# Kernel tuning notes

Measured on AMD Instinct MI355X. Metric: run time of the kernel, lower is better.

The kernel has to match this reference:

```python
import jax, jax.numpy as jnp
import numpy as np

N, E = 50000, 800000
IN, C, H, EDIM = 128, 16, 8, 8  # in_channels, out_channels per head, heads, edge_dim
NEG_SLOPE = 0.2


def setup_inputs() -> dict:
    key = jax.random.key(0)
    ks = jax.random.split(key, 10)
    g = 1.0 / np.sqrt(IN)
    inp = {
        "x": jax.random.normal(ks[0], (N, IN), dtype=jnp.float32),
        "edge_index": jax.random.randint(ks[1], (2, E), 0, N, dtype=jnp.int64),
        "edge_attr": jax.random.normal(ks[2], (E, EDIM), dtype=jnp.float32),
        # GATv2Conv params (share_weights=False): lin_l, lin_r with bias, lin_edge no bias
        "W_l": jax.random.normal(ks[3], (IN, H * C), dtype=jnp.float32) * g,
        "b_l": jnp.zeros((H * C,), dtype=jnp.float32),
        "W_r": jax.random.normal(ks[4], (IN, H * C), dtype=jnp.float32) * g,
        "b_r": jnp.zeros((H * C,), dtype=jnp.float32),
        "W_e": jax.random.normal(ks[5], (EDIM, H * C), dtype=jnp.float32) * (1.0 / np.sqrt(EDIM)),
        "att": jax.random.normal(ks[6], (H, C), dtype=jnp.float32) * (1.0 / np.sqrt(C)),
        "bias": jnp.zeros((H * C,), dtype=jnp.float32),
    }
    return inp


def _gatv2_forward(x, edge_index, edge_attr, W_l, b_l, W_r, b_r, W_e, att, bias):
    n = x.shape[0]
    x_l = (x @ W_l + b_l).reshape(n, H, C)  # source transform
    x_r = (x @ W_r + b_r).reshape(n, H, C)  # target transform

    # add self-loops; edge_attr fill_value='mean' (PyG GATv2Conv default)
    loop = jnp.arange(n, dtype=edge_index.dtype)
    src = jnp.concatenate([edge_index[0], loop])
    dst = jnp.concatenate([edge_index[1], loop])
    loop_attr = jnp.broadcast_to(edge_attr.mean(axis=0, keepdims=True), (n, EDIM))
    e_attr = jnp.concatenate([edge_attr, loop_attr], axis=0)  # [E+N, EDIM]

    e_emb = (e_attr @ W_e).reshape(-1, H, C)  # [E+N, H, C]
    m = x_l[src] + x_r[dst] + e_emb          # gather per edge
    m = jax.nn.leaky_relu(m, NEG_SLOPE)
    logit = jnp.einsum("ehc,hc->eh", m, att)  # [E+N, H]

    # destination-grouped (scatter) softmax
    seg_max = jax.ops.segment_max(logit, dst, num_segments=n)
    expd = jnp.exp(logit - seg_max[dst])
    seg_sum = jax.ops.segment_sum(expd, dst, num_segments=n)
    alpha = expd / (seg_sum[dst] + 1e-16)     # [E+N, H]

    msg = alpha[:, :, None] * x_l[src]        # [E+N, H, C]
    out = jax.ops.segment_sum(msg, dst, num_segments=n)  # [N, H, C]
    return out.reshape(n, H * C) + bias       # concat heads + bias


def reference(x, edge_index, edge_attr, W_l, b_l, W_r, b_r, W_e, att, bias):
    return _gatv2_forward(x, edge_index, edge_attr, W_l, b_l, W_r, b_r, W_e, att, bias)
```

## Files before the change

### kernel.cpp

```cpp
#include <hip/hip_runtime.h>

#define NHEAD 8
#define CH    16
#define HC    128
#define INC   128
#define EDIM  8
#define NEG   0.2f

typedef _Float16 h8 __attribute__((ext_vector_type(8)));
typedef _Float16 h4 __attribute__((ext_vector_type(4)));
typedef _Float16 h2 __attribute__((ext_vector_type(2)));
typedef float    f4 __attribute__((ext_vector_type(4)));

__device__ __forceinline__ float lrelu(float v) { return v > 0.f ? v : NEG * v; }

__global__ void k_loop_emb(const float* __restrict__ attr_sum, const float* __restrict__ We,
                           const float* __restrict__ att, float* __restrict__ loop_emb,
                           _Float16* __restrict__ We16, _Float16* __restrict__ att16,
                           float invE) {
    int j = threadIdx.x;
    float acc = 0.f;
    #pragma unroll
    for (int d = 0; d < EDIM; ++d) {
        float w = We[d * HC + j];
        acc += attr_sum[d] * invE * w;
        We16[d * HC + j] = (_Float16)w;
    }
    loop_emb[j] = acc;
    att16[j] = (_Float16)att[j];
}

__global__ void k_packW(const float* __restrict__ Wl, const float* __restrict__ Wr,
                        _Float16* __restrict__ packed) {
    int id = blockIdx.x * blockDim.x + threadIdx.x;
    int l  = id & 63;
    int kb = (id >> 6) & 3;
    int t  = id >> 8;
    int col = t * 16 + (l & 15);
    const float* W = (col < HC) ? Wl : Wr;
    int c = col & 127;
    int kbase = kb * 32 + (l >> 4) * 8;
    _Float16* dst = packed + (size_t)id * 8;
    #pragma unroll
    for (int j = 0; j < 8; ++j) dst[j] = (_Float16)W[(size_t)(kbase + j) * HC + c];
}

__global__ __launch_bounds__(256) void k_gemm_mfma(
        const float* __restrict__ x, const _Float16* __restrict__ packed,
        const float* __restrict__ bl, const float* __restrict__ br,
        _Float16* __restrict__ xh, int N) {
    int nb0 = blockIdx.x * 128;
    int w  = threadIdx.x >> 6;
    int l  = threadIdx.x & 63;

    const h8* pk = (const h8*)packed;
    h8 bfrag[4][4];
    #pragma unroll
    for (int t4 = 0; t4 < 4; ++t4)
        #pragma unroll
        for (int kb = 0; kb < 4; ++kb)
            bfrag[t4][kb] = pk[(size_t)(((w * 4 + t4) * 4 + kb) * 64 + l)];

    float bv[4];
    int cl = l & 15;
    #pragma unroll
    for (int t4 = 0; t4 < 4; ++t4) {
        int col = w * 64 + t4 * 16 + cl;
        bv[t4] = (col < HC) ? bl[col] : br[col - HC];
    }

    int g = l >> 4;
    int r0 = g * 4;
    for (int mt = 0; mt < 8; ++mt) {
        int m0 = nb0 + mt * 16;
        if (m0 >= N) break;
        int row = m0 + cl; if (row >= N) row = N - 1;
        const float* xp = x + (size_t)row * INC + g * 8;
        h8 afrag[4];
        #pragma unroll
        for (int kb = 0; kb < 4; ++kb) {
            float4 u = *(const float4*)(xp + kb * 32);
            float4 v = *(const float4*)(xp + kb * 32 + 4);
            h8 a;
            a[0] = (_Float16)u.x; a[1] = (_Float16)u.y; a[2] = (_Float16)u.z; a[3] = (_Float16)u.w;
            a[4] = (_Float16)v.x; a[5] = (_Float16)v.y; a[6] = (_Float16)v.z; a[7] = (_Float16)v.w;
            afrag[kb] = a;
        }
        f4 acc[4];
        #pragma unroll
        for (int t4 = 0; t4 < 4; ++t4) { f4 z = {0.f, 0.f, 0.f, 0.f}; acc[t4] = z; }
        #pragma unroll
        for (int kb = 0; kb < 4; ++kb)
            #pragma unroll
            for (int t4 = 0; t4 < 4; ++t4)
                acc[t4] = __builtin_amdgcn_mfma_f32_16x16x32_f16(afrag[kb], bfrag[t4][kb], acc[t4], 0, 0, 0);
        #pragma unroll
        for (int t4 = 0; t4 < 4; ++t4) {
            int col = w * 64 + t4 * 16 + cl;
            #pragma unroll
            for (int j = 0; j < 4; ++j) {
                int node = m0 + r0 + j;
                if (node < N) xh[(size_t)node * 256 + col] = (_Float16)(acc[t4][j] + bv[t4]);
            }
        }
    }
}

__global__ void k_hist(const int* __restrict__ ei, int* __restrict__ cnt, int E) {
    int t = blockIdx.x * blockDim.x + threadIdx.x;
    if (t < E) atomicAdd(&cnt[ei[E + t]], 1);
}

__global__ void k_scan1(const int* __restrict__ cnt, int* __restrict__ off,
                        int* __restrict__ bsum, int N) {
    __shared__ int wpre[16];
    int i = blockIdx.x * 1024 + threadIdx.x;
    int lane = threadIdx.x & 63, wid = threadIdx.x >> 6;
    int v = (i < N) ? cnt[i] : 0;
    int s = v;
    #pragma unroll
    for (int d = 1; d < 64; d <<= 1) {
        int t = __shfl_up(s, d);
        if (lane >= d) s += t;
    }
    if (lane == 63) wpre[wid] = s;
    __syncthreads();
    if (threadIdx.x == 0) {
        int run = 0;
        #pragma unroll
        for (int q = 0; q < 16; ++q) { int t = wpre[q]; wpre[q] = run; run += t; }
        bsum[blockIdx.x] = run;
    }
    __syncthreads();
    if (i < N) off[i] = wpre[wid] + s - v;
}

__global__ void k_scan2(const int* __restrict__ bsum, int* __restrict__ bsx,
                        int* __restrict__ offN, int nb) {
    int lane = threadIdx.x;
    int v = (lane < nb) ? bsum[lane] : 0;
    int s = v;
    #pragma unroll
    for (int d = 1; d < 64; d <<= 1) {
        int t = __shfl_up(s, d);
        if (lane >= d) s += t;
    }
    if (lane < nb) bsx[lane] = s - v;
    if (lane == 63) *offN = s;
}

__global__ void k_scan3(int* __restrict__ off, const int* __restrict__ bsx, int N) {
    int i = blockIdx.x * 1024 + threadIdx.x;
    if (i < N) off[i] += bsx[blockIdx.x];
}

__global__ void k_scatter(const int* __restrict__ ei, const float* __restrict__ ea,
                          const int* __restrict__ off, int* __restrict__ cur,
                          int* __restrict__ esrc, h8* __restrict__ eac,
                          float* __restrict__ attr_sum, int E) {
    __shared__ float red[4][8];
    int t = blockIdx.x * blockDim.x + threadIdx.x;
    float av[8] = {0.f, 0.f, 0.f, 0.f, 0.f, 0.f, 0.f, 0.f};
    if (t < E) {
        int dst = ei[E + t];
        int pos = off[dst] + atomicAdd(&cur[dst], 1);
        esrc[pos] = ei[t];
        float4 a0 = *(const float4*)(ea + (size_t)t * EDIM);
        float4 a1 = *(const float4*)(ea + (size_t)t * EDIM + 4);
        av[0] = a0.x; av[1] = a0.y; av[2] = a0.z; av[3] = a0.w;
        av[4] = a1.x; av[5] = a1.y; av[6] = a1.z; av[7] = a1.w;
        h8 v;
        #pragma unroll
        for (int k = 0; k < 8; ++k) v[k] = (_Float16)av[k];
        eac[pos] = v;
    }
    #pragma unroll
    for (int m = 1; m < 64; m <<= 1) {
        #pragma unroll
        for (int k = 0; k < 8; ++k) av[k] += __shfl_xor(av[k], m);
    }
    int lane = threadIdx.x & 63, wid = threadIdx.x >> 6;
    if (lane == 0) {
        #pragma unroll
        for (int k = 0; k < 8; ++k) red[wid][k] = av[k];
    }
    __syncthreads();
    if (threadIdx.x < 8) {
        float s = red[0][threadIdx.x] + red[1][threadIdx.x] + red[2][threadIdx.x] + red[3][threadIdx.x];
        atomicAdd(&attr_sum[threadIdx.x], s);
    }
}

__global__ void k_gather(const int* __restrict__ esrc, const h8* __restrict__ eac,
                         const _Float16* __restrict__ We16, const _Float16* __restrict__ att16,
                         const float* __restrict__ att,
                         const _Float16* __restrict__ xh,
                         const float* __restrict__ loop_emb, const float* __restrict__ bias,
                         const int* __restrict__ off, float* __restrict__ out, int N) {
    int wave = (blockIdx.x * blockDim.x + threadIdx.x) >> 6;
    int lane = threadIdx.x & 63;
    if (wave >= N) return;
    int dst = __builtin_amdgcn_readfirstlane(wave);
    int half = lane >> 5;
    int l = lane & 31;
    int c0 = l * 4;

    h4 we4[EDIM];
    #pragma unroll
    for (int d = 0; d < EDIM; ++d) we4[d] = *(const h4*)(We16 + d * HC + c0);
    h2 attlo = *(const h2*)(att16 + c0);
    h2 atthi = *(const h2*)(att16 + c0 + 2);
    h4 xr4 = *(const h4*)(xh + (size_t)dst * 256 + HC + c0);
    float xr0 = (float)xr4[0], xr1 = (float)xr4[1], xr2f = (float)xr4[2], xr3 = (float)xr4[3];

    float acc0 = 0.f, acc1 = 0.f, acc2 = 0.f, acc3 = 0.f, segw = 0.f;

    {
        h4 xl4 = *(const h4*)(xh + (size_t)dst * 256 + c0);
        float x0 = (float)xl4[0], x1 = (float)xl4[1], x2 = (float)xl4[2], x3 = (float)xl4[3];
        float4 le = *(const float4*)(loop_emb + c0);
        float4 af = *(const float4*)(att + c0);
        float m0 = lrelu(x0 + xr0 + le.x);
        float m1 = lrelu(x1 + xr1 + le.y);
        float m2 = lrelu(x2 + xr2f + le.z);
        float m3 = lrelu(x3 + xr3 + le.w);
        float p = m0 * af.x + m1 * af.y + m2 * af.z + m3 * af.w;
        p += __shfl_xor(p, 1); p += __shfl_xor(p, 2);
        float w = half ? 0.f : __expf(p);
        segw += w; acc0 += w * x0; acc1 += w * x1; acc2 += w * x2; acc3 += w * x3;
    }

    int beg = off[dst], end = off[dst + 1];
    if (beg < end) {
        const h2 ng2 = {(_Float16)NEG, (_Float16)NEG};
        const h4 z4 = {};
        h4 ng4; ng4[0] = ng2[0]; ng4[1] = ng2[0]; ng4[2] = ng2[0]; ng4[3] = ng2[0];
        int j1 = beg + half;     if (j1 >= end) j1 = end - 1;
        int j2 = beg + 2 + half; if (j2 >= end) j2 = end - 1;
        int src1 = esrc[j1]; h8 a1 = eac[j1];
        int src2 = esrc[j2]; h8 a2 = eac[j2];
        h4 xl1 = *(const h4*)(xh + (size_t)src1 * 256 + c0);
        for (int i = beg; i < end; i += 2) {
            bool valid = (i + half) < end;
            h8 a8 = a1; h4 xl4 = xl1;
            a1 = a2; src1 = src2;
            xl1 = *(const h4*)(xh + (size_t)src1 * 256 + c0);
            int in4 = i + 4;
            if (in4 < end) {
                int jn = in4 + half; if (jn >= end) jn = end - 1;
                src2 = esrc[jn]; a2 = eac[jn];
            }
            h4 e4 = {};
            #pragma unroll
            for (int d = 0; d < EDIM; ++d) {
                h4 ad; ad[0] = a8[d]; ad[1] = a8[d]; ad[2] = a8[d]; ad[3] = a8[d];
                e4 += ad * we4[d];
            }
            h4 m4 = xl4 + xr4 + e4;
            h4 mp = __builtin_elementwise_max(m4, z4);
            h4 mn = __builtin_elementwise_min(m4, z4);
            m4 = mp + mn * ng4;
            h2 mlo; mlo[0] = m4[0]; mlo[1] = m4[1];
            h2 mhi; mhi[0] = m4[2]; mhi[1] = m4[3];
#if __has_builtin(__builtin_amdgcn_fdot2)
            float p = __builtin_amdgcn_fdot2(mlo, attlo, 0.f, false);
            p = __builtin_amdgcn_fdot2(mhi, atthi, p, false);
#else
            float p = (float)m4[0] * (float)attlo[0] + (float)m4[1] * (float)attlo[1]
                    + (float)m4[2] * (float)atthi[0] + (float)m4[3] * (float)atthi[1];
#endif
            p += __shfl_xor(p, 1);
            p += __shfl_xor(p, 2);
            float w = valid ? __expf(p) : 0.f;
            segw += w;
            acc0 += w * (float)xl4[0];
            acc1 += w * (float)xl4[1];
            acc2 += w * (float)xl4[2];
            acc3 += w * (float)xl4[3];
        }
    }

    segw += __shfl_xor(segw, 32);
    acc0 += __shfl_xor(acc0, 32);
    acc1 += __shfl_xor(acc1, 32);
    acc2 += __shfl_xor(acc2, 32);
    acc3 += __shfl_xor(acc3, 32);

    if (half == 0) {
        float inv = 1.f / (segw + 1e-16f);
        float4 bv = *(const float4*)(bias + c0);
        float4 o;
        o.x = acc0 * inv + bv.x;
        o.y = acc1 * inv + bv.y;
        o.z = acc2 * inv + bv.z;
        o.w = acc3 * inv + bv.w;
        *(float4*)(out + (size_t)dst * HC + c0) = o;
    }
}

extern "C" void kernel_launch(void* const* d_in, const int* in_sizes, int n_in,
                              void* d_out, int out_size, void* d_ws, size_t ws_size,
                              hipStream_t stream) {
    int N = in_sizes[0] / INC;
    int E = in_sizes[1] / 2;
    const float* x    = (const float*)d_in[0];
    const int*   ei   = (const int*)d_in[1];
    const float* ea   = (const float*)d_in[2];
    const float* Wl   = (const float*)d_in[3];
    const float* bl   = (const float*)d_in[4];
    const float* Wr   = (const float*)d_in[5];
    const float* br   = (const float*)d_in[6];
    const float* We   = (const float*)d_in[7];
    const float* att  = (const float*)d_in[8];
    const float* bias = (const float*)d_in[9];
    float* out = (float*)d_out;

    _Float16* xh      = (_Float16*)d_ws;
    h8*       eac     = (h8*)(xh + (size_t)N * 256);
    float* attr_sum   = (float*)(eac + E);
    int*   cnt        = (int*)(attr_sum + 8);
    int*   cur        = cnt + N;
    float* loop_emb   = (float*)(cur + N);
    _Float16* packed  = (_Float16*)(loop_emb + HC);
    _Float16* We16    = packed + 32768;
    _Float16* att16   = We16 + 1024;
    int*   off        = (int*)(att16 + 128);
    int*   esrc       = off + (N + 1);
    int*   bsum       = esrc + E;
    int*   bsx        = bsum + 64;

    hipMemsetAsync(attr_sum, 0, (8 + 2 * (size_t)N) * sizeof(float), stream);

    k_packW<<<16, 256, 0, stream>>>(Wl, Wr, packed);
    k_gemm_mfma<<<(N + 127) / 128, 256, 0, stream>>>(x, packed, bl, br, xh, N);

    k_hist<<<(E + 255) / 256, 256, 0, stream>>>(ei, cnt, E);
    int nb = (N + 1023) / 1024;
    k_scan1<<<nb, 1024, 0, stream>>>(cnt, off, bsum, N);
    k_scan2<<<1, 64, 0, stream>>>(bsum, bsx, off + N, nb);
    k_scan3<<<nb, 1024, 0, stream>>>(off, bsx, N);
    k_scatter<<<(E + 255) / 256, 256, 0, stream>>>(ei, ea, off, cur, esrc, eac, attr_sum, E);

    k_loop_emb<<<1, HC, 0, stream>>>(attr_sum, We, att, loop_emb, We16, att16, 1.0f / (float)E);

    k_gather<<<(N * 64 + 255) / 256, 256, 0, stream>>>(esrc, eac, We16, att16, att, xh,
                                                       loop_emb, bias, off, out, N);
}
```

Baseline: 198.8 us.

## Stage GEMM output via LDS, reuse hist ranks, drop scan3, deepen gather prefetch

The GEMM epilogue now stages fp16 results in shared memory and writes them as 16-byte row-contiguous stores instead of scattered 2-byte stores. The histogram kernel records each edge's atomic rank, so the scatter no longer needs a second atomic pass or the cursor array. The third scan kernel is removed and consumers add the block prefix on the fly. The gather loop prefetches one more edge ahead to hide latency on the indirect loads. The cost is an extra E-sized rank array plus two more barriers per GEMM tile.

```diff
diff --git a/kernel.cpp b/kernel.cpp
--- a/kernel.cpp
+++ b/kernel.cpp
@@ -49,6 +49,7 @@
         const float* __restrict__ x, const _Float16* __restrict__ packed,
         const float* __restrict__ bl, const float* __restrict__ br,
         _Float16* __restrict__ xh, int N) {
+    __shared__ _Float16 st[16][264];
     int nb0 = blockIdx.x * 128;
     int w  = threadIdx.x >> 6;
     int l  = threadIdx.x & 63;
@@ -98,17 +99,25 @@
         for (int t4 = 0; t4 < 4; ++t4) {
             int col = w * 64 + t4 * 16 + cl;
             #pragma unroll
-            for (int j = 0; j < 4; ++j) {
-                int node = m0 + r0 + j;
-                if (node < N) xh[(size_t)node * 256 + col] = (_Float16)(acc[t4][j] + bv[t4]);
-            }
+            for (int j = 0; j < 4; ++j)
+                st[r0 + j][col] = (_Float16)(acc[t4][j] + bv[t4]);
         }
-    }
-}
-
-__global__ void k_hist(const int* __restrict__ ei, int* __restrict__ cnt, int E) {
+        __syncthreads();
+        #pragma unroll
+        for (int q = 0; q < 2; ++q) {
+            int cch = threadIdx.x + 256 * q;
+            int r = cch >> 5, ch = (cch & 31) * 8;
+            int node = m0 + r;
+            if (node < N) *(h8*)(xh + (size_t)node * 256 + ch) = *(const h8*)&st[r][ch];
+        }
+        __syncthreads();
+    }
+}
+
+__global__ void k_hist(const int* __restrict__ ei, int* __restrict__ cnt,
+                       int* __restrict__ rank, int E) {
     int t = blockIdx.x * blockDim.x + threadIdx.x;
-    if (t < E) atomicAdd(&cnt[ei[E + t]], 1);
+    if (t < E) rank[t] = atomicAdd(&cnt[ei[E + t]], 1);
 }
 
 __global__ void k_scan1(const int* __restrict__ cnt, int* __restrict__ off,
@@ -132,11 +141,10 @@
         bsum[blockIdx.x] = run;
     }
     __syncthreads();
-    if (i < N) off[i] = wpre[wid] + s - v;
-}
-
-__global__ void k_scan2(const int* __restrict__ bsum, int* __restrict__ bsx,
-                        int* __restrict__ offN, int nb) {
+    if (i <= N) off[i] = wpre[wid] + s - v;
+}
+
+__global__ void k_scan2(const int* __restrict__ bsum, int* __restrict__ bsx, int nb) {
     int lane = threadIdx.x;
     int v = (lane < nb) ? bsum[lane] : 0;
     int s = v;
@@ -146,16 +154,11 @@
         if (lane >= d) s += t;
     }
     if (lane < nb) bsx[lane] = s - v;
-    if (lane == 63) *offN = s;
-}
-
-__global__ void k_scan3(int* __restrict__ off, const int* __restrict__ bsx, int N) {
-    int i = blockIdx.x * 1024 + threadIdx.x;
-    if (i < N) off[i] += bsx[blockIdx.x];
 }
 
 __global__ void k_scatter(const int* __restrict__ ei, const float* __restrict__ ea,
-                          const int* __restrict__ off, int* __restrict__ cur,
+                          const int* __restrict__ off, const int* __restrict__ bsx,
+                          const int* __restrict__ rank,
                           int* __restrict__ esrc, h8* __restrict__ eac,
                           float* __restrict__ attr_sum, int E) {
     __shared__ float red[4][8];
@@ -163,7 +166,7 @@
     float av[8] = {0.f, 0.f, 0.f, 0.f, 0.f, 0.f, 0.f, 0.f};
     if (t < E) {
         int dst = ei[E + t];
-        int pos = off[dst] + atomicAdd(&cur[dst], 1);
+        int pos = off[dst] + bsx[dst >> 10] + rank[t];
         esrc[pos] = ei[t];
         float4 a0 = *(const float4*)(ea + (size_t)t * EDIM);
         float4 a1 = *(const float4*)(ea + (size_t)t * EDIM + 4);
@@ -196,7 +199,8 @@
                          const float* __restrict__ att,
                          const _Float16* __restrict__ xh,
                          const float* __restrict__ loop_emb, const float* __restrict__ bias,
-                         const int* __restrict__ off, float* __restrict__ out, int N) {
+                         const int* __restrict__ off, const int* __restrict__ bsx,
+                         float* __restrict__ out, int N) {
     int wave = (blockIdx.x * blockDim.x + threadIdx.x) >> 6;
     int lane = threadIdx.x & 63;
     if (wave >= N) return;
@@ -230,33 +234,32 @@
         segw += w; acc0 += w * x0; acc1 += w * x1; acc2 += w * x2; acc3 += w * x3;
     }
 
-    int beg = off[dst], end = off[dst + 1];
+    int beg = off[dst] + bsx[dst >> 10];
+    int end = off[dst + 1] + bsx[(dst + 1) >> 10];
     if (beg < end) {
-        const h2 ng2 = {(_Float16)NEG, (_Float16)NEG};
         const h4 z4 = {};
-        h4 ng4; ng4[0] = ng2[0]; ng4[1] = ng2[0]; ng4[2] = ng2[0]; ng4[3] = ng2[0];
-        int j1 = beg + half;     if (j1 >= end) j1 = end - 1;
-        int j2 = beg + 2 + half; if (j2 >= end) j2 = end - 1;
-        int src1 = esrc[j1]; h8 a1 = eac[j1];
-        int src2 = esrc[j2]; h8 a2 = eac[j2];
-        h4 xl1 = *(const h4*)(xh + (size_t)src1 * 256 + c0);
+        h4 ng4; ng4[0] = (_Float16)NEG; ng4[1] = (_Float16)NEG; ng4[2] = (_Float16)NEG; ng4[3] = (_Float16)NEG;
+        int last = end - 1;
+        int j0 = beg + half;     if (j0 > last) j0 = last;
+        int j1 = beg + 2 + half; if (j1 > last) j1 = last;
+        int j2 = beg + 4 + half; if (j2 > last) j2 = last;
+        int sA = esrc[j0]; h8 aA = eac[j0];
+        int sB = esrc[j1]; h8 aB = eac[j1];
+        int sC = esrc[j2]; h8 aC = eac[j2];
+        h4 xlA = *(const h4*)(xh + (size_t)sA * 256 + c0);
+        h4 xlB = *(const h4*)(xh + (size_t)sB * 256 + c0);
         for (int i = beg; i < end; i += 2) {
+            h4 xlC = *(const h4*)(xh + (size_t)sC * 256 + c0);
+            int j3 = i + 6 + half; if (j3 > last) j3 = last;
+            int sD = esrc[j3]; h8 aD = eac[j3];
             bool valid = (i + half) < end;
-            h8 a8 = a1; h4 xl4 = xl1;
-            a1 = a2; src1 = src2;
-            xl1 = *(const h4*)(xh + (size_t)src1 * 256 + c0);
-            int in4 = i + 4;
-            if (in4 < end) {
-                int jn = in4 + half; if (jn >= end) jn = end - 1;
-                src2 = esrc[jn]; a2 = eac[jn];
-            }
             h4 e4 = {};
             #pragma unroll
             for (int d = 0; d < EDIM; ++d) {
-                h4 ad; ad[0] = a8[d]; ad[1] = a8[d]; ad[2] = a8[d]; ad[3] = a8[d];
+                h4 ad; ad[0] = aA[d]; ad[1] = aA[d]; ad[2] = aA[d]; ad[3] = aA[d];
                 e4 += ad * we4[d];
             }
-            h4 m4 = xl4 + xr4 + e4;
+            h4 m4 = xlA + xr4 + e4;
             h4 mp = __builtin_elementwise_max(m4, z4);
             h4 mn = __builtin_elementwise_min(m4, z4);
             m4 = mp + mn * ng4;
@@ -273,10 +276,13 @@
             p += __shfl_xor(p, 2);
             float w = valid ? __expf(p) : 0.f;
             segw += w;
-            acc0 += w * (float)xl4[0];
-            acc1 += w * (float)xl4[1];
-            acc2 += w * (float)xl4[2];
-            acc3 += w * (float)xl4[3];
+            acc0 += w * (float)xlA[0];
+            acc1 += w * (float)xlA[1];
+            acc2 += w * (float)xlA[2];
+            acc3 += w * (float)xlA[3];
+            aA = aB; aB = aC; aC = aD;
+            xlA = xlB; xlB = xlC;
+            sC = sD;
         }
     }
 
@@ -319,30 +325,29 @@
     h8*       eac     = (h8*)(xh + (size_t)N * 256);
     float* attr_sum   = (float*)(eac + E);
     int*   cnt        = (int*)(attr_sum + 8);
-    int*   cur        = cnt + N;
-    float* loop_emb   = (float*)(cur + N);
+    float* loop_emb   = (float*)(cnt + N);
     _Float16* packed  = (_Float16*)(loop_emb + HC);
     _Float16* We16    = packed + 32768;
     _Float16* att16   = We16 + 1024;
     int*   off        = (int*)(att16 + 128);
-    int*   esrc       = off + (N + 1);
+    int*   rank       = off + (N + 2);
+    int*   esrc       = rank + E;
     int*   bsum       = esrc + E;
     int*   bsx        = bsum + 64;
 
-    hipMemsetAsync(attr_sum, 0, (8 + 2 * (size_t)N) * sizeof(float), stream);
+    hipMemsetAsync(attr_sum, 0, (8 + (size_t)N) * sizeof(float), stream);
 
     k_packW<<<16, 256, 0, stream>>>(Wl, Wr, packed);
     k_gemm_mfma<<<(N + 127) / 128, 256, 0, stream>>>(x, packed, bl, br, xh, N);
 
-    k_hist<<<(E + 255) / 256, 256, 0, stream>>>(ei, cnt, E);
-    int nb = (N + 1023) / 1024;
+    k_hist<<<(E + 255) / 256, 256, 0, stream>>>(ei, cnt, rank, E);
+    int nb = (N + 1 + 1023) / 1024;
     k_scan1<<<nb, 1024, 0, stream>>>(cnt, off, bsum, N);
-    k_scan2<<<1, 64, 0, stream>>>(bsum, bsx, off + N, nb);
-    k_scan3<<<nb, 1024, 0, stream>>>(off, bsx, N);
-    k_scatter<<<(E + 255) / 256, 256, 0, stream>>>(ei, ea, off, cur, esrc, eac, attr_sum, E);
+    k_scan2<<<1, 64, 0, stream>>>(bsum, bsx, nb);
+    k_scatter<<<(E + 255) / 256, 256, 0, stream>>>(ei, ea, off, bsx, rank, esrc, eac, attr_sum, E);
 
     k_loop_emb<<<1, HC, 0, stream>>>(attr_sum, We, att, loop_emb, We16, att16, 1.0f / (float)E);
 
     k_gather<<<(N * 64 + 255) / 256, 256, 0, stream>>>(esrc, eac, We16, att16, att, xh,
-                                                       loop_emb, bias, off, out, N);
-}
+                                                       loop_emb, bias, off, bsx, out, N);
+}
```

Result: faster. 187.9 us (-5.5%).
